# Optimization experiments

Measured on AMD Instinct MI355X. Metric: run time of the kernel, lower is better.

## Reference

```python
import jax, jax.numpy as jnp
import numpy as np

UNITS = 1024
N_CLASSES = 41
SUBSAMPLE = 4
KERNEL = 3
FEAT = 256


def setup_inputs() -> dict:
    key = jax.random.key(0)
    ks = jax.random.split(key, 12)
    B, T, F, U, C = 32, 1000, FEAT, UNITS, N_CLASSES
    s = lambda k, shape, sc: jax.random.normal(k, shape, dtype=jnp.float32) * sc
    return {
        "x": jax.random.normal(ks[0], (B, T, F), dtype=jnp.float32),
        # depthwise conv kernel: (width, 1, channels) for WIO with groups=C
        "conv_w": s(ks[1], (KERNEL, 1, F), 0.1),
        "h0_init": s(ks[2], (1, U), 0.05),
        "w0_x": s(ks[3], (F, 3 * U), 1.0 / np.sqrt(F)),
        "w0_h": s(ks[4], (U, 3 * U), 1.0 / np.sqrt(U)),
        "b0": jnp.zeros((2, 3 * U), dtype=jnp.float32),
        "w1_x": s(ks[5], (U, 3 * U), 1.0 / np.sqrt(U)),
        "w1_h": s(ks[6], (U, 3 * U), 1.0 / np.sqrt(U)),
        "b1": jnp.zeros((2, 3 * U), dtype=jnp.float32),
        "dense_w": s(ks[7], (U, C), 1.0 / np.sqrt(U)),
        "dense_b": jnp.zeros((C,), dtype=jnp.float32),
    }


def _depthwise_conv1d(x, w):
    # x: [B, T, C], w: [K, 1, C]; SAME padding, groups = C, relu, no bias
    C = x.shape[-1]
    y = jax.lax.conv_general_dilated(
        x, w, window_strides=(1,), padding="SAME",
        dimension_numbers=("NWC", "WIO", "NWC"), feature_group_count=C)
    return jax.nn.relu(y)


def _gru_layer(x, h0, Wx, Wh, b):
    # Keras GRU v2 (reset_after=True), gate order z, r, h.
    # x: [B, T, F]; h0: [B, U]; Wx: [F, 3U]; Wh: [U, 3U]; b: [2, 3U]
    xproj = jnp.einsum("btf,fg->btg", x, Wx) + b[0]  # [B, T, 3U]
    br = b[1]

    def step(h, xp):
        rec = h @ Wh + br  # [B, 3U]
        xz, xr, xh = jnp.split(xp, 3, axis=-1)
        rz, rr, rh = jnp.split(rec, 3, axis=-1)
        z = jax.nn.sigmoid(xz + rz)
        r = jax.nn.sigmoid(xr + rr)
        hh = jnp.tanh(xh + r * rh)
        hn = z * h + (1.0 - z) * hh
        return hn, hn

    _, ys = jax.lax.scan(step, h0, jnp.swapaxes(xproj, 0, 1))  # [T, B, U]
    return jnp.swapaxes(ys, 0, 1)


def reference(x, conv_w, h0_init, w0_x, w0_h, b0, w1_x, w1_h, b1, dense_w, dense_b):
    B = x.shape[0]
    U = w0_h.shape[0]
    h = _depthwise_conv1d(x, conv_w)
    # layer 0: learned initial state tiled over batch
    h = _gru_layer(h, jnp.tile(h0_init, (B, 1)), w0_x, w0_h, b0)
    # subsample after layer nLayers-2 == 0
    h = h[:, ::SUBSAMPLE, :]
    # layer 1: zero initial state (Keras default when initial_state is None)
    h = _gru_layer(h, jnp.zeros((B, U), dtype=x.dtype), w1_x, w1_h, b1)
    return h @ dense_w + dense_b  # [B, T//4, nClasses]
```

## Files before the change

kernel.cpp:

```cpp
#include <hip/hip_runtime.h>

typedef unsigned int u32;
typedef unsigned long long u64;
typedef unsigned short u16;
typedef __attribute__((ext_vector_type(8))) short short8;
typedef __attribute__((ext_vector_type(4))) float f32x4;
typedef __attribute__((ext_vector_type(4))) unsigned int u32x4;

#define MFMA(a,b,c) __builtin_amdgcn_mfma_f32_16x16x32_bf16((a),(b),(c),0,0,0)
#define ALOAD32(p)    __hip_atomic_load((p), __ATOMIC_RELAXED, __HIP_MEMORY_SCOPE_AGENT)
#define ASTORE32(p,v) __hip_atomic_store((p),(v), __ATOMIC_RELAXED, __HIP_MEMORY_SCOPE_AGENT)

__device__ __forceinline__ float bf2f(u32 b){ union{u32 u; float f;} v; v.u = b<<16; return v.f; }
__device__ __forceinline__ u16 f2bf(float f){ union{float f; u32 u;} v; v.f = f; u32 u = v.u;
  return (u16)((u + 0x7fffu + ((u>>16)&1u)) >> 16); }
__device__ __forceinline__ u32 pack_f(float v){
  u16 hi = f2bf(v); u16 lo = f2bf(v - bf2f(hi)); return (u32)hi | ((u32)lo<<16); }

__device__ __forceinline__ void unpack8(uint4 a, uint4 b, short8& hi, short8& lo){
  u32 w[8] = {a.x,a.y,a.z,a.w,b.x,b.y,b.z,b.w};
#pragma unroll
  for (int j=0;j<8;++j){ hi[j] = (short)(w[j] & 0xffffu); lo[j] = (short)(w[j] >> 16); }
}
__device__ __forceinline__ void unpackh4(u32x4 a, short8& hi){
#pragma unroll
  for (int i=0;i<4;++i){ hi[2*i] = (short)(a[i] & 0xffffu); hi[2*i+1] = (short)(a[i] >> 16); }
}

constexpr size_t OFF_Y    = 0;
constexpr size_t OFF_SUB  = 32768000;
constexpr size_t OFF_W0IH = 65536000;
constexpr size_t OFF_W0IL = 73400320;
constexpr size_t OFF_W1XH = 81264640;
constexpr size_t OFF_W1XL = 87556096;
constexpr size_t OFF_W1HH = 93847552;
constexpr size_t OFF_W1HL = 100139008;
constexpr size_t OFF_HB0  = 106430464;
constexpr size_t OFF_HB1  = 106692608;
constexpr size_t OFF_FL0  = 106954752;
constexpr size_t OFF_FL1  = 106955776;
constexpr size_t WS_NEED  = 106956800;

__global__ void build_frags(const float* __restrict__ W, u16* __restrict__ fhi,
                            u16* __restrict__ flo, int K){
  const int KT = K >> 8;
  size_t total = (size_t)K * 12 * 256;
  for (size_t i = (size_t)blockIdx.x*blockDim.x + threadIdx.x; i < total;
       i += (size_t)gridDim.x*blockDim.x){
    int j = (int)(i & 7); size_t r = i >> 3;
    int c = (int)(r % 12); r /= 12;
    int kseg = (int)(r & 3); r >>= 2;
    int kt = (int)(r % KT); r /= KT;
    int kq = (int)(r & 7); r >>= 3;
    int wg = (int)r;
    int k = kq*(K>>3) + kt*32 + kseg*8 + j;
    int col = (c>>2)*1024 + wg*4 + (c&3);
    float v = W[(size_t)k*3072 + col];
    u16 hi = f2bf(v);
    u16 lo = f2bf(v - bf2f(hi));
    fhi[i] = hi; flo[i] = lo;
  }
}

__global__ void build_w0img(const float* __restrict__ w0x, const float* __restrict__ w0h,
                            u16* __restrict__ imgH, u16* __restrict__ imgL){
  for (size_t i = (size_t)blockIdx.x*blockDim.x + threadIdx.x; i < 128ull*30720ull;
       i += (size_t)gridDim.x*blockDim.x){
    int wg = (int)(i / 30720), e = (int)(i % 30720);
    int k, col; const float* src;
    if (e < 4096){
      int blk=e>>9, r=e&511, kseg=r>>7, c=(r>>3)&15, j=r&7;
      k = blk*32 + kseg*8 + j;
      col = (c<8) ? (wg*8+c) : (1024 + wg*8 + c-8); src = w0x;
    } else if (e < 20480){
      int e2=e-4096, blk=e2>>9, r=e2&511, kseg=r>>7, c=(r>>3)&15, j=r&7;
      k = blk*32 + kseg*8 + j;
      col = (c<8) ? (wg*8+c) : (1024 + wg*8 + c-8); src = w0h;
    } else if (e < 24576){
      int e2=e-20480, blk=e2>>9, r=e2&511, kseg=r>>7, c=(r>>3)&15, j=r&7;
      k = blk*32 + kseg*8 + j;
      if (c < 8){ col = 2048 + wg*8 + c;     src = w0x; }
      else      { col = 2048 + wg*8 + c - 8; src = w0h; }
    } else {
      int e2=e-24576, blk=e2>>8, r=e2&255, kseg=r>>6, c=(r>>3)&7, j=r&7;
      k = 256 + blk*32 + kseg*8 + j;
      col = 2048 + wg*8 + c; src = w0h;
    }
    float v = src[(size_t)k*3072 + col];
    u16 hi = f2bf(v);
    imgH[i] = hi; imgL[i] = f2bf(v - bf2f(hi));
  }
}

__global__ void init_state(const float* __restrict__ h0, u32* hb0, u32* hb1,
                           int* f0, int* f1){
  int i = blockIdx.x*blockDim.x + threadIdx.x;
  if (i < 256){ f0[i]=0; f1[i]=0; }
  if (i < 16384){
    int p = i & 511;
    u32 v = (u32)f2bf(h0[2*p]) | ((u32)f2bf(h0[2*p+1]) << 16);
    hb0[i] = v;
    hb1[i] = 0u;
  }
}

__global__ void conv_pack(const float* __restrict__ x, const float* __restrict__ cw,
                          u32* __restrict__ yp){
  for (size_t i = (size_t)blockIdx.x*blockDim.x + threadIdx.x; i < 8192000ull;
       i += (size_t)gridDim.x*blockDim.x){
    int f = (int)(i & 255); int b = (int)((i>>8)&31); int t = (int)(i>>13);
    const float* xb = x + ((size_t)b*1000 + t)*256 + f;
    float acc = xb[0]*cw[256+f];
    if (t > 0)   acc += xb[-256]*cw[f];
    if (t < 999) acc += xb[256]*cw[512+f];
    acc = fmaxf(acc, 0.0f);
    yp[i] = pack_f(acc);
  }
}

__global__ __launch_bounds__(512, 1)
void gru8s_persist(const u32* __restrict__ xin,
                   const u16* __restrict__ imgH, const u16* __restrict__ imgL,
                   const float* __restrict__ bias,
                   u32* hbuf, int* flags, u32* out_pack)
{
  __shared__ u16 WIMG[45056];
  __shared__ float exch[128*33];
  __shared__ float harr[128];
  __shared__ int hready[32];

  const int tid  = threadIdx.x;
  const int wg   = blockIdx.x;
  const int g    = wg >> 7;
  const int wid  = wg & 127;
  const int lane = tid & 63;
  const int wave = tid >> 6;
  const int kq   = wave;
  const int lo16 = lane & 15, hi16 = lane >> 4;
  const int lane_off = hi16*128 + lo16*8;
  const int hsel = (kq >= 4) ? 16 : 0;

  {
    const u64* sH = (const u64*)(imgH + (size_t)wid*30720);
    const u64* sL = (const u64*)(imgL + (size_t)wid*30720 + 4096);
    u64* dH = (u64*)WIMG;
    u64* dL = (u64*)(WIMG + 24576);
    for (int i = tid; i < 6144; i += 512) dH[i] = sH[i];
    for (int i = tid; i < 5120; i += 512) dL[i] = sL[i];
    if (tid < 32) hready[tid] = 0;
    if (tid < 128){
      u16 hv = ((const u16*)hbuf)[g*16384 + (tid>>3)*1024 + wid*8 + (tid&7)];
      harr[tid] = bf2f((u32)hv);
    }
  }
  __syncthreads();

  const u16* zrx_h  = &WIMG[kq*512 + lane_off];
  const u16* zrxg_l = imgL + (size_t)wid*30720 + kq*512 + lane_off;
  const u16* zrh_h  = &WIMG[4096 + kq*2048 + lane_off];
  const u16* hhx_h  = &WIMG[20480 + kq*512 + lane_off];
  const bool hhLds  = (kq < 2);
  const u16* hhb_h; const u16* hhb_l; int hhstride;
  if (hhLds){
    hhb_h = &WIMG[20480 + kq*2048 + lane_off]; hhb_l = hhb_h + 20480; hhstride = 512;
  } else {
    size_t go = (size_t)wid*30720 + 24576 + (size_t)(kq-2)*1024 + hi16*64
              + ((lo16 >= 8) ? (lo16-8)*8 : 0);
    hhb_h = imgH + go; hhb_l = imgL + go; hhstride = 256;
  }

  const int gs = tid >> 3, gu = tid & 7, eu = wid*8 + gu;
  const float zb  = bias[eu]        + bias[3072 + eu];
  const float rbv = bias[1024 + eu] + bias[4096 + eu];
  const float hxb = bias[2048 + eu];
  const float hrb = bias[5120 + eu];

  for (int t = 0; t < 1000; ++t) {
    const int cur = t & 1, nxt = cur ^ 1;
    f32x4 aZR = (f32x4){0.f,0.f,0.f,0.f};
    f32x4 aHX = (f32x4){0.f,0.f,0.f,0.f};
    f32x4 aHR = (f32x4){0.f,0.f,0.f,0.f};
    {
      const u32* xr = xin + ((size_t)t*32 + g*16 + lo16)*256 + kq*32 + hi16*8;
      uint4 a0 = *(const uint4*)xr;
      uint4 a1 = *(const uint4*)(xr + 4);
      short8 ahi, alo; unpack8(a0, a1, ahi, alo);
      short8 b1h = *(const short8*)zrx_h, b1l = *(const short8*)zrxg_l;
      short8 b2h = *(const short8*)hhx_h, b2l = *(const short8*)(hhx_h + 20480);
      aZR = MFMA(ahi,b1h,aZR); aZR = MFMA(alo,b1h,aZR); aZR = MFMA(ahi,b1l,aZR);
      aHX = MFMA(ahi,b2h,aHX); aHX = MFMA(alo,b2h,aHX); aHX = MFMA(ahi,b2l,aHX);
    }
    if (t > 0) {
      if (wave == 0) {
        int f0;
        do { f0 = ALOAD32(flags + g*128 + lane); } while (__all(f0 >= t) == 0);
        asm volatile("" ::: "memory");
        if (lane == 0) ((volatile int*)hready)[0] = t;
      } else if (wave == 1) {
        int f1;
        do { f1 = ALOAD32(flags + g*128 + 64 + lane); } while (__all(f1 >= t) == 0);
        asm volatile("" ::: "memory");
        if (lane == 0) ((volatile int*)hready)[16] = t;
      }
      while (((volatile int*)hready)[hsel] < t) { }
      asm volatile("" ::: "memory");
    }
    {
      const u32* hrow = hbuf + cur*16384 + g*8192 + lo16*512 + kq*64 + hi16*4;
      u32x4 qa, qb, qc, qd;
      asm volatile(
        "global_load_dwordx4 %0, %4, off sc0 sc1\n\t"
        "global_load_dwordx4 %1, %4, off offset:64 sc0 sc1\n\t"
        "global_load_dwordx4 %2, %4, off offset:128 sc0 sc1\n\t"
        "global_load_dwordx4 %3, %4, off offset:192 sc0 sc1\n\t"
        "s_waitcnt vmcnt(0)"
        : "=&v"(qa), "=&v"(qb), "=&v"(qc), "=&v"(qd)
        : "v"(hrow)
        : "memory");
      short8 ah0, ah1, ah2, ah3;
      unpackh4(qa, ah0); unpackh4(qb, ah1); unpackh4(qc, ah2); unpackh4(qd, ah3);
      {
        short8 b1h = *(const short8*)(zrh_h + 0*512);
        short8 b1l = *(const short8*)(zrh_h + 0*512 + 20480);
        short8 b2h = *(const short8*)(hhb_h + 0*hhstride);
        short8 b2l = *(const short8*)(hhb_l + 0*hhstride);
        aZR = MFMA(ah0,b1h,aZR); aZR = MFMA(ah0,b1l,aZR);
        aHR = MFMA(ah0,b2h,aHR); aHR = MFMA(ah0,b2l,aHR);
      }
      {
        short8 b1h = *(const short8*)(zrh_h + 1*512);
        short8 b1l = *(const short8*)(zrh_h + 1*512 + 20480);
        short8 b2h = *(const short8*)(hhb_h + 1*hhstride);
        short8 b2l = *(const short8*)(hhb_l + 1*hhstride);
        aZR = MFMA(ah1,b1h,aZR); aZR = MFMA(ah1,b1l,aZR);
        aHR = MFMA(ah1,b2h,aHR); aHR = MFMA(ah1,b2l,aHR);
      }
      {
        short8 b1h = *(const short8*)(zrh_h + 2*512);
        short8 b1l = *(const short8*)(zrh_h + 2*512 + 20480);
        short8 b2h = *(const short8*)(hhb_h + 2*hhstride);
        short8 b2l = *(const short8*)(hhb_l + 2*hhstride);
        aZR = MFMA(ah2,b1h,aZR); aZR = MFMA(ah2,b1l,aZR);
        aHR = MFMA(ah2,b2h,aHR); aHR = MFMA(ah2,b2l,aHR);
      }
      {
        short8 b1h = *(const short8*)(zrh_h + 3*512);
        short8 b1l = *(const short8*)(zrh_h + 3*512 + 20480);
        short8 b2h = *(const short8*)(hhb_h + 3*hhstride);
        short8 b2l = *(const short8*)(hhb_l + 3*hhstride);
        aZR = MFMA(ah3,b1h,aZR); aZR = MFMA(ah3,b1l,aZR);
        aHR = MFMA(ah3,b2h,aHR); aHR = MFMA(ah3,b2l,aHR);
      }
    }
    {
      const int bb = hi16*4;
#pragma unroll
      for (int r4 = 0; r4 < 4; ++r4){
        exch[(kq*16 + bb + r4)*33 + lo16]      = aZR[r4];
        exch[(kq*16 + bb + r4)*33 + 16 + lo16] = (lo16 < 8) ? aHX[r4] : aHR[r4];
      }
    }
    __syncthreads();
    u32 pk_out = 0;
    if (tid < 128) {
      float zp=0.f, rp=0.f, xh=0.f, rh=0.f;
#pragma unroll
      for (int k8 = 0; k8 < 8; ++k8){
        const float* e = &exch[(k8*16 + gs)*33];
        zp += e[gu]; rp += e[8+gu]; xh += e[16+gu]; rh += e[24+gu];
      }
      float z = 1.f/(1.f + __expf(-(zp + zb)));
      float r = 1.f/(1.f + __expf(-(rp + rbv)));
      float pre = xh + hxb + r*(rh + hrb);
      float ex = __expf(-2.f*fabsf(pre));
      float th = (1.f - ex)/(1.f + ex);
      float hh = copysignf(th, pre);
      float hn = z*harr[tid] + (1.f - z)*hh;
      harr[tid] = hn;
      pk_out = pack_f(hn);
      int pk16 = (int)(pk_out & 0xffffu);
      int prt  = __shfl_xor(pk16, 1);
      if ((tid & 1) == 0) {
        u32 pair = (u32)pk16 | ((u32)prt << 16);
        ASTORE32(hbuf + nxt*16384 + g*8192 + gs*512 + wid*4 + (gu>>1), pair);
      }
    }
    asm volatile("s_waitcnt vmcnt(0)" ::: "memory");
    __syncthreads();
    if (tid == 0)
      ASTORE32(flags + g*128 + wid, t+1);
    if (tid < 128) {
      if ((t & 3) == 0)
        out_pack[((size_t)(t>>2)*32 + g*16 + gs)*1024 + eu] = pk_out;
    }
  }
}

template<int LAYER>
__global__ __launch_bounds__(1024, 1)
void gru_persist(const u32* __restrict__ xin,
                 const u16* __restrict__ wxf_hi, const u16* __restrict__ wxf_lo,
                 const u16* __restrict__ whf_hi, const u16* __restrict__ whf_lo,
                 const float* __restrict__ bias,
                 u32* hbuf, int* flags, u32* out_pack)
{
  constexpr int T   = (LAYER==0) ? 1000 : 250;
  constexpr int KX  = (LAYER==0) ? 256 : 1024;
  constexpr int KTX = KX >> 8;
  __shared__ u16 WxHi[8*KTX*512], WxLo[8*KTX*512];
  __shared__ u16 WhHi[8*4*512],  WhLo[8*4*512];
  __shared__ float exch[8*32*18];
  __shared__ float harr[128];
  __shared__ int hready[32];

  const int tid  = threadIdx.x;
  const int wg   = blockIdx.x;
  const int lane = tid & 63;
  const int wave = tid >> 6;
  const int m    = wave & 1;
  const int kq   = wave >> 1;
  const int u0   = wg * 4;
  const int lo16 = lane & 15, hi16 = lane >> 4;
  const int lane_off = hi16*128 + lo16*8;
  const int hsel = (kq >= 4) ? 16 : 0;

  {
    for (int i = tid; i < 8*KTX*512/4; i += 1024){ ((u64*)WxHi)[i]=0; ((u64*)WxLo)[i]=0; }
    for (int i = tid; i < 8*4*512/4;  i += 1024){ ((u64*)WhHi)[i]=0; ((u64*)WhLo)[i]=0; }
    if (tid < 32) hready[tid] = 0;
  }
  __syncthreads();
  {
    const u16* bx_hi = wxf_hi + (size_t)wg*KX*12;
    const u16* bx_lo = wxf_lo + (size_t)wg*KX*12;
    const u16* bh_hi = whf_hi + (size_t)wg*1024*12;
    const u16* bh_lo = whf_lo + (size_t)wg*1024*12;
    for (int i = tid; i < 8*KTX*48; i += 1024){
      int c = i % 12; int r = i/12; int kseg = r & 3; r >>= 2;
      int kt = r % KTX; int kqq = r / KTX;
      int ldsoff = ((kqq*KTX+kt)*4+kseg)*128 + c*8;
      *(short8*)&WxHi[ldsoff] = *(const short8*)&bx_hi[(size_t)i*8];
      *(short8*)&WxLo[ldsoff] = *(const short8*)&bx_lo[(size_t)i*8];
    }
    for (int i = tid; i < 8*4*48; i += 1024){
      int c = i % 12; int r = i/12; int kseg = r & 3; r >>= 2;
      int kt = r & 3; int kqq = r >> 2;
      int cm = (c < 8) ? c : (c + 4);
      int ldsoff = ((kqq*4+kt)*4+kseg)*128 + cm*8;
      *(short8*)&WhHi[ldsoff] = *(const short8*)&bh_hi[(size_t)i*8];
      *(short8*)&WhLo[ldsoff] = *(const short8*)&bh_lo[(size_t)i*8];
    }
    if (tid < 128){
      u16 hv = ((const u16*)hbuf)[(tid>>2)*1024 + u0 + (tid&3)];
      harr[tid] = bf2f((u32)hv);
    }
  }
  __syncthreads();

  const int eb = tid >> 2, eu_l = tid & 3, eu = u0 + eu_l;
  const float zb  = bias[eu]        + bias[3072 + eu];
  const float rbv = bias[1024 + eu] + bias[4096 + eu];
  const float hxb = bias[2048 + eu];
  const float hrb = bias[5120 + eu];

  for (int t = 0; t < T; ++t) {
    const int cur = t & 1, nxt = cur ^ 1;
    f32x4 xacc = (f32x4){0.f,0.f,0.f,0.f};
    f32x4 racc = (f32x4){0.f,0.f,0.f,0.f};
    {
      const u32* xrow = xin + ((size_t)t*32 + 16*m + lo16)*KX + kq*(KX>>3) + hi16*8;
#pragma unroll
      for (int kt = 0; kt < KTX; ++kt) {
        uint4 a0 = *(const uint4*)(xrow + kt*32);
        uint4 a1 = *(const uint4*)(xrow + kt*32 + 4);
        short8 ahi, alo; unpack8(a0, a1, ahi, alo);
        short8 bhi = *(const short8*)&WxHi[(kq*KTX+kt)*512 + lane_off];
        short8 blo = *(const short8*)&WxLo[(kq*KTX+kt)*512 + lane_off];
        xacc = MFMA(ahi, bhi, xacc);
        xacc = MFMA(alo, bhi, xacc);
        xacc = MFMA(ahi, blo, xacc);
      }
    }
    if (t > 0) {
      if (wave == 0) {
        int f0, f1;
        do { f0 = ALOAD32(flags + lane); f1 = ALOAD32(flags + 64 + lane); }
        while (!__all(f0 >= t && f1 >= t));
        asm volatile("" ::: "memory");
        if (lane == 0) ((volatile int*)hready)[0] = t;
      } else if (wave == 1) {
        int f2, f3;
        do { f2 = ALOAD32(flags + 128 + lane); f3 = ALOAD32(flags + 192 + lane); }
        while (!__all(f2 >= t && f3 >= t));
        asm volatile("" ::: "memory");
        if (lane == 0) ((volatile int*)hready)[16] = t;
      }
      while (((volatile int*)hready)[hsel] < t) { }
      asm volatile("" ::: "memory");
    }
    {
      const u32* hrow = hbuf + cur*16384 + (16*m + lo16)*512 + kq*64 + hi16*4;
      u32x4 qa, qb, qc, qd;
      asm volatile(
        "global_load_dwordx4 %0, %4, off sc0 sc1\n\t"
        "global_load_dwordx4 %1, %4, off offset:64 sc0 sc1\n\t"
        "global_load_dwordx4 %2, %4, off offset:128 sc0 sc1\n\t"
        "global_load_dwordx4 %3, %4, off offset:192 sc0 sc1\n\t"
        "s_waitcnt vmcnt(0)"
        : "=&v"(qa), "=&v"(qb), "=&v"(qc), "=&v"(qd)
        : "v"(hrow)
        : "memory");
      short8 ah0, ah1, ah2, ah3;
      unpackh4(qa, ah0); unpackh4(qb, ah1); unpackh4(qc, ah2); unpackh4(qd, ah3);
      {
        short8 bhi = *(const short8*)&WhHi[(kq*4+0)*512 + lane_off];
        short8 blo = *(const short8*)&WhLo[(kq*4+0)*512 + lane_off];
        racc = MFMA(ah0, bhi, racc); racc = MFMA(ah0, blo, racc);
      }
      {
        short8 bhi = *(const short8*)&WhHi[(kq*4+1)*512 + lane_off];
        short8 blo = *(const short8*)&WhLo[(kq*4+1)*512 + lane_off];
        racc = MFMA(ah1, bhi, racc); racc = MFMA(ah1, blo, racc);
      }
      {
        short8 bhi = *(const short8*)&WhHi[(kq*4+2)*512 + lane_off];
        short8 blo = *(const short8*)&WhLo[(kq*4+2)*512 + lane_off];
        racc = MFMA(ah2, bhi, racc); racc = MFMA(ah2, blo, racc);
      }
      {
        short8 bhi = *(const short8*)&WhHi[(kq*4+3)*512 + lane_off];
        short8 blo = *(const short8*)&WhLo[(kq*4+3)*512 + lane_off];
        racc = MFMA(ah3, bhi, racc); racc = MFMA(ah3, blo, racc);
      }
    }
    {
      const int bb = 16*m + hi16*4;
#pragma unroll
      for (int r4 = 0; r4 < 4; ++r4)
        exch[(kq*32 + bb + r4)*18 + lo16] = xacc[r4] + racc[r4];
    }
    __syncthreads();
    u32 pk_out = 0;
    if (tid < 128) {
      float zp=0.f, rp=0.f, xh=0.f, rh=0.f;
#pragma unroll
      for (int qd = 0; qd < 8; ++qd) {
        const float* e = &exch[(qd*32 + eb)*18];
        zp += e[eu_l];
        rp += e[4 + eu_l];
        xh += e[8 + eu_l];
        rh += e[12 + eu_l];
      }
      float z = 1.f/(1.f + __expf(-(zp + zb)));
      float r = 1.f/(1.f + __expf(-(rp + rbv)));
      float pre = xh + hxb + r*(rh + hrb);
      float ex = __expf(-2.f*fabsf(pre));
      float th = (1.f - ex)/(1.f + ex);
      float hh = copysignf(th, pre);
      float hn = z*harr[tid] + (1.f - z)*hh;
      harr[tid] = hn;
      pk_out = pack_f(hn);
      int pk16 = (int)(pk_out & 0xffffu);
      int prt  = __shfl_xor(pk16, 1);
      if ((tid & 1) == 0) {
        u32 pair = (u32)pk16 | ((u32)prt << 16);
        ASTORE32(hbuf + nxt*16384 + eb*512 + wg*2 + (eu_l>>1), pair);
      }
    }
    asm volatile("s_waitcnt vmcnt(0)" ::: "memory");
    __syncthreads();
    if (tid == 0)
      ASTORE32(flags + wg, t+1);
    if (tid < 128) {
      if (LAYER==0) {
        if ((t & 3) == 0)
          out_pack[((size_t)(t>>2)*32 + eb)*1024 + u0 + eu_l] = pk_out;
      } else {
        out_pack[((size_t)t*32 + eb)*1024 + u0 + eu_l] = pk_out;
      }
    }
  }
}

__global__ __launch_bounds__(256, 1)
void dense_k(const u32* __restrict__ h2, const float* __restrict__ W,
             const float* __restrict__ bias, float* __restrict__ out){
  __shared__ float rows[32*1025];
  const int ts = blockIdx.x;
  const u32* src = h2 + (size_t)ts*32768;
  for (int i = threadIdx.x; i < 32768; i += 256){
    u32 p = src[i];
    rows[(i>>10)*1025 + (i&1023)] = bf2f(p & 0xffffu) + bf2f(p >> 16);
  }
  __syncthreads();
  const int b = threadIdx.x >> 3, cg = threadIdx.x & 7;
  float acc[6] = {0.f,0.f,0.f,0.f,0.f,0.f};
  for (int k = 0; k < 1024; ++k){
    float hv = rows[b*1025 + k];
    const float* wr = W + k*41;
#pragma unroll
    for (int j = 0; j < 6; ++j){ int c = cg + 8*j; if (c < 41) acc[j] += hv*wr[c]; }
  }
#pragma unroll
  for (int j = 0; j < 6; ++j){
    int c = cg + 8*j;
    if (c < 41) out[((size_t)b*250 + ts)*41 + c] = acc[j] + bias[c];
  }
}

extern "C" void kernel_launch(void* const* d_in, const int* in_sizes, int n_in,
                              void* d_out, int out_size, void* d_ws, size_t ws_size,
                              hipStream_t stream) {
  const float* x      = (const float*)d_in[0];
  const float* conv_w = (const float*)d_in[1];
  const float* h0i    = (const float*)d_in[2];
  const float* w0x    = (const float*)d_in[3];
  const float* w0h    = (const float*)d_in[4];
  const float* b0     = (const float*)d_in[5];
  const float* w1x    = (const float*)d_in[6];
  const float* w1h    = (const float*)d_in[7];
  const float* b1     = (const float*)d_in[8];
  const float* dw     = (const float*)d_in[9];
  const float* db     = (const float*)d_in[10];
  float* outp = (float*)d_out;

  if (ws_size < WS_NEED) return;

  char* ws = (char*)d_ws;
  u32* y_pack   = (u32*)(ws + OFF_Y);
  u32* out2     = (u32*)(ws + OFF_Y);
  u32* sub_pack = (u32*)(ws + OFF_SUB);
  u16* w0iH = (u16*)(ws + OFF_W0IH); u16* w0iL = (u16*)(ws + OFF_W0IL);
  u16* w1x_hi = (u16*)(ws + OFF_W1XH); u16* w1x_lo = (u16*)(ws + OFF_W1XL);
  u16* w1h_hi = (u16*)(ws + OFF_W1HH); u16* w1h_lo = (u16*)(ws + OFF_W1HL);
  u32* hb0 = (u32*)(ws + OFF_HB0);
  u32* hb1 = (u32*)(ws + OFF_HB1);
  int* fl0 = (int*)(ws + OFF_FL0);
  int* fl1 = (int*)(ws + OFF_FL1);

  init_state<<<64, 512, 0, stream>>>(h0i, hb0, hb1, fl0, fl1);
  build_w0img<<<2048, 256, 0, stream>>>(w0x, w0h, w0iH, w0iL);
  build_frags<<<2048, 256, 0, stream>>>(w1x, w1x_hi, w1x_lo, 1024);
  build_frags<<<2048, 256, 0, stream>>>(w1h, w1h_hi, w1h_lo, 1024);
  conv_pack<<<4096, 256, 0, stream>>>(x, conv_w, y_pack);

  gru8s_persist<<<256, 512, 0, stream>>>(y_pack, w0iH, w0iL, b0, hb0, fl0, sub_pack);
  gru_persist<1><<<256, 1024, 0, stream>>>(sub_pack, w1x_hi, w1x_lo, w1h_hi, w1h_lo,
                                           b1, hb1, fl1, out2);

  dense_k<<<250, 256, 0, stream>>>(out2, dw, db, outp);
}
```

Before: 5.990 ms.

## Repartition layer-0 GRU into 4 batch groups of 8 with 16 units per block

The layer-0 persistent GRU now splits the batch into four groups of 8 sequences, and each block owns 16 hidden units instead of 8. Z, R and H gates each get a full 16-column MFMA tile, and the weight image is rebuilt in a matching layout. Only the hi halves go to LDS; the lo halves are now always read from global memory. The intent is to cut the number of blocks each one synchronises with per step (64 instead of 128) and to raise per-block work. The cost is that half of each 16-row MFMA is wasted on duplicated batch rows and there is more global traffic for the lo weights.

```diff
diff --git a/kernel.cpp b/kernel.cpp
--- a/kernel.cpp
+++ b/kernel.cpp
@@ -64,28 +64,20 @@
 
 __global__ void build_w0img(const float* __restrict__ w0x, const float* __restrict__ w0h,
                             u16* __restrict__ imgH, u16* __restrict__ imgL){
-  for (size_t i = (size_t)blockIdx.x*blockDim.x + threadIdx.x; i < 128ull*30720ull;
+  for (size_t i = (size_t)blockIdx.x*blockDim.x + threadIdx.x; i < 64ull*61440ull;
        i += (size_t)gridDim.x*blockDim.x){
-    int wg = (int)(i / 30720), e = (int)(i % 30720);
-    int k, col; const float* src;
-    if (e < 4096){
-      int blk=e>>9, r=e&511, kseg=r>>7, c=(r>>3)&15, j=r&7;
-      k = blk*32 + kseg*8 + j;
-      col = (c<8) ? (wg*8+c) : (1024 + wg*8 + c-8); src = w0x;
-    } else if (e < 20480){
-      int e2=e-4096, blk=e2>>9, r=e2&511, kseg=r>>7, c=(r>>3)&15, j=r&7;
-      k = blk*32 + kseg*8 + j;
-      col = (c<8) ? (wg*8+c) : (1024 + wg*8 + c-8); src = w0h;
-    } else if (e < 24576){
-      int e2=e-20480, blk=e2>>9, r=e2&511, kseg=r>>7, c=(r>>3)&15, j=r&7;
-      k = blk*32 + kseg*8 + j;
-      if (c < 8){ col = 2048 + wg*8 + c;     src = w0x; }
-      else      { col = 2048 + wg*8 + c - 8; src = w0h; }
-    } else {
-      int e2=e-24576, blk=e2>>8, r=e2&255, kseg=r>>6, c=(r>>3)&7, j=r&7;
-      k = 256 + blk*32 + kseg*8 + j;
-      col = 2048 + wg*8 + c; src = w0h;
-    }
+    int wid = (int)(i / 61440), e = (int)(i % 61440);
+    int e2, colbase; const float* src;
+    if      (e < 4096) { e2 = e;         colbase = 0;    src = w0x; }
+    else if (e < 8192) { e2 = e - 4096;  colbase = 1024; src = w0x; }
+    else if (e < 24576){ e2 = e - 8192;  colbase = 0;    src = w0h; }
+    else if (e < 40960){ e2 = e - 24576; colbase = 1024; src = w0h; }
+    else if (e < 45056){ e2 = e - 40960; colbase = 2048; src = w0x; }
+    else               { e2 = e - 45056; colbase = 2048; src = w0h; }
+    int blk = e2 >> 9, r = e2 & 511;
+    int kseg = r >> 7, c = (r >> 3) & 15, j = r & 7;
+    int k = blk*32 + kseg*8 + j;
+    int col = colbase + wid*16 + c;
     float v = src[(size_t)k*3072 + col];
     u16 hi = f2bf(v);
     imgH[i] = hi; imgL[i] = f2bf(v - bf2f(hi));
@@ -119,57 +111,49 @@
 }
 
 __global__ __launch_bounds__(512, 1)
-void gru8s_persist(const u32* __restrict__ xin,
+void gru16_persist(const u32* __restrict__ xin,
                    const u16* __restrict__ imgH, const u16* __restrict__ imgL,
                    const float* __restrict__ bias,
                    u32* hbuf, int* flags, u32* out_pack)
 {
-  __shared__ u16 WIMG[45056];
-  __shared__ float exch[128*33];
+  __shared__ u16 WIMG[61440];
+  __shared__ float exch[8*8*66];
   __shared__ float harr[128];
   __shared__ int hready[32];
 
   const int tid  = threadIdx.x;
   const int wg   = blockIdx.x;
-  const int g    = wg >> 7;
-  const int wid  = wg & 127;
+  const int g    = wg >> 6;
+  const int wid  = wg & 63;
   const int lane = tid & 63;
   const int wave = tid >> 6;
   const int kq   = wave;
   const int lo16 = lane & 15, hi16 = lane >> 4;
   const int lane_off = hi16*128 + lo16*8;
   const int hsel = (kq >= 4) ? 16 : 0;
+  const int srow = lo16 & 7;
 
   {
-    const u64* sH = (const u64*)(imgH + (size_t)wid*30720);
-    const u64* sL = (const u64*)(imgL + (size_t)wid*30720 + 4096);
+    const u64* sH = (const u64*)(imgH + (size_t)wid*61440);
     u64* dH = (u64*)WIMG;
-    u64* dL = (u64*)(WIMG + 24576);
-    for (int i = tid; i < 6144; i += 512) dH[i] = sH[i];
-    for (int i = tid; i < 5120; i += 512) dL[i] = sL[i];
+    for (int i = tid; i < 15360; i += 512) dH[i] = sH[i];
     if (tid < 32) hready[tid] = 0;
     if (tid < 128){
-      u16 hv = ((const u16*)hbuf)[g*16384 + (tid>>3)*1024 + wid*8 + (tid&7)];
+      u16 hv = ((const u16*)hbuf)[g*8192 + (tid>>4)*1024 + wid*16 + (tid&15)];
       harr[tid] = bf2f((u32)hv);
     }
   }
   __syncthreads();
 
-  const u16* zrx_h  = &WIMG[kq*512 + lane_off];
-  const u16* zrxg_l = imgL + (size_t)wid*30720 + kq*512 + lane_off;
-  const u16* zrh_h  = &WIMG[4096 + kq*2048 + lane_off];
-  const u16* hhx_h  = &WIMG[20480 + kq*512 + lane_off];
-  const bool hhLds  = (kq < 2);
-  const u16* hhb_h; const u16* hhb_l; int hhstride;
-  if (hhLds){
-    hhb_h = &WIMG[20480 + kq*2048 + lane_off]; hhb_l = hhb_h + 20480; hhstride = 512;
-  } else {
-    size_t go = (size_t)wid*30720 + 24576 + (size_t)(kq-2)*1024 + hi16*64
-              + ((lo16 >= 8) ? (lo16-8)*8 : 0);
-    hhb_h = imgH + go; hhb_l = imgL + go; hhstride = 256;
-  }
-
-  const int gs = tid >> 3, gu = tid & 7, eu = wid*8 + gu;
+  const u16* gLo  = imgL + (size_t)wid*61440;
+  const u16* zx_h = &WIMG[kq*512 + lane_off];          const u16* zx_l = gLo + kq*512 + lane_off;
+  const u16* rx_h = &WIMG[4096 + kq*512 + lane_off];   const u16* rx_l = gLo + 4096 + kq*512 + lane_off;
+  const u16* zh_h = &WIMG[8192 + kq*2048 + lane_off];  const u16* zh_l = gLo + 8192 + kq*2048 + lane_off;
+  const u16* rh_h = &WIMG[24576 + kq*2048 + lane_off]; const u16* rh_l = gLo + 24576 + kq*2048 + lane_off;
+  const u16* xh_h = &WIMG[40960 + kq*512 + lane_off];  const u16* xh_l = gLo + 40960 + kq*512 + lane_off;
+  const u16* hh_h = &WIMG[45056 + kq*2048 + lane_off]; const u16* hh_l = gLo + 45056 + kq*2048 + lane_off;
+
+  const int gs = tid >> 4, gu = tid & 15, eu = wid*16 + gu;
   const float zb  = bias[eu]        + bias[3072 + eu];
   const float rbv = bias[1024 + eu] + bias[4096 + eu];
   const float hxb = bias[2048 + eu];
@@ -177,28 +161,31 @@
 
   for (int t = 0; t < 1000; ++t) {
     const int cur = t & 1, nxt = cur ^ 1;
-    f32x4 aZR = (f32x4){0.f,0.f,0.f,0.f};
+    f32x4 aZ  = (f32x4){0.f,0.f,0.f,0.f};
+    f32x4 aR  = (f32x4){0.f,0.f,0.f,0.f};
     f32x4 aHX = (f32x4){0.f,0.f,0.f,0.f};
     f32x4 aHR = (f32x4){0.f,0.f,0.f,0.f};
     {
-      const u32* xr = xin + ((size_t)t*32 + g*16 + lo16)*256 + kq*32 + hi16*8;
+      const u32* xr = xin + ((size_t)t*32 + g*8 + srow)*256 + kq*32 + hi16*8;
       uint4 a0 = *(const uint4*)xr;
       uint4 a1 = *(const uint4*)(xr + 4);
       short8 ahi, alo; unpack8(a0, a1, ahi, alo);
-      short8 b1h = *(const short8*)zrx_h, b1l = *(const short8*)zrxg_l;
-      short8 b2h = *(const short8*)hhx_h, b2l = *(const short8*)(hhx_h + 20480);
-      aZR = MFMA(ahi,b1h,aZR); aZR = MFMA(alo,b1h,aZR); aZR = MFMA(ahi,b1l,aZR);
-      aHX = MFMA(ahi,b2h,aHX); aHX = MFMA(alo,b2h,aHX); aHX = MFMA(ahi,b2l,aHX);
+      short8 bzh = *(const short8*)zx_h, bzl = *(const short8*)zx_l;
+      short8 brh = *(const short8*)rx_h, brl = *(const short8*)rx_l;
+      short8 bxh = *(const short8*)xh_h, bxl = *(const short8*)xh_l;
+      aZ  = MFMA(ahi,bzh,aZ);  aZ  = MFMA(alo,bzh,aZ);  aZ  = MFMA(ahi,bzl,aZ);
+      aR  = MFMA(ahi,brh,aR);  aR  = MFMA(alo,brh,aR);  aR  = MFMA(ahi,brl,aR);
+      aHX = MFMA(ahi,bxh,aHX); aHX = MFMA(alo,bxh,aHX); aHX = MFMA(ahi,bxl,aHX);
     }
     if (t > 0) {
       if (wave == 0) {
         int f0;
-        do { f0 = ALOAD32(flags + g*128 + lane); } while (__all(f0 >= t) == 0);
+        do { f0 = ALOAD32(flags + g*64 + (lane & 31)); } while (__all(f0 >= t) == 0);
         asm volatile("" ::: "memory");
         if (lane == 0) ((volatile int*)hready)[0] = t;
       } else if (wave == 1) {
         int f1;
-        do { f1 = ALOAD32(flags + g*128 + 64 + lane); } while (__all(f1 >= t) == 0);
+        do { f1 = ALOAD32(flags + g*64 + 32 + (lane & 31)); } while (__all(f1 >= t) == 0);
         asm volatile("" ::: "memory");
         if (lane == 0) ((volatile int*)hready)[16] = t;
       }
@@ -206,7 +193,7 @@
       asm volatile("" ::: "memory");
     }
     {
-      const u32* hrow = hbuf + cur*16384 + g*8192 + lo16*512 + kq*64 + hi16*4;
+      const u32* hrow = hbuf + cur*16384 + g*4096 + srow*512 + kq*64 + hi16*4;
       u32x4 qa, qb, qc, qd;
       asm volatile(
         "global_load_dwordx4 %0, %4, off sc0 sc1\n\t"
@@ -219,45 +206,27 @@
         : "memory");
       short8 ah0, ah1, ah2, ah3;
       unpackh4(qa, ah0); unpackh4(qb, ah1); unpackh4(qc, ah2); unpackh4(qd, ah3);
-      {
-        short8 b1h = *(const short8*)(zrh_h + 0*512);
-        short8 b1l = *(const short8*)(zrh_h + 0*512 + 20480);
-        short8 b2h = *(const short8*)(hhb_h + 0*hhstride);
-        short8 b2l = *(const short8*)(hhb_l + 0*hhstride);
-        aZR = MFMA(ah0,b1h,aZR); aZR = MFMA(ah0,b1l,aZR);
-        aHR = MFMA(ah0,b2h,aHR); aHR = MFMA(ah0,b2l,aHR);
-      }
-      {
-        short8 b1h = *(const short8*)(zrh_h + 1*512);
-        short8 b1l = *(const short8*)(zrh_h + 1*512 + 20480);
-        short8 b2h = *(const short8*)(hhb_h + 1*hhstride);
-        short8 b2l = *(const short8*)(hhb_l + 1*hhstride);
-        aZR = MFMA(ah1,b1h,aZR); aZR = MFMA(ah1,b1l,aZR);
-        aHR = MFMA(ah1,b2h,aHR); aHR = MFMA(ah1,b2l,aHR);
-      }
-      {
-        short8 b1h = *(const short8*)(zrh_h + 2*512);
-        short8 b1l = *(const short8*)(zrh_h + 2*512 + 20480);
-        short8 b2h = *(const short8*)(hhb_h + 2*hhstride);
-        short8 b2l = *(const short8*)(hhb_l + 2*hhstride);
-        aZR = MFMA(ah2,b1h,aZR); aZR = MFMA(ah2,b1l,aZR);
-        aHR = MFMA(ah2,b2h,aHR); aHR = MFMA(ah2,b2l,aHR);
-      }
-      {
-        short8 b1h = *(const short8*)(zrh_h + 3*512);
-        short8 b1l = *(const short8*)(zrh_h + 3*512 + 20480);
-        short8 b2h = *(const short8*)(hhb_h + 3*hhstride);
-        short8 b2l = *(const short8*)(hhb_l + 3*hhstride);
-        aZR = MFMA(ah3,b1h,aZR); aZR = MFMA(ah3,b1l,aZR);
-        aHR = MFMA(ah3,b2h,aHR); aHR = MFMA(ah3,b2l,aHR);
+#pragma unroll
+      for (int kt = 0; kt < 4; ++kt){
+        short8 ah = (kt==0)?ah0:(kt==1)?ah1:(kt==2)?ah2:ah3;
+        short8 bzh = *(const short8*)(zh_h + kt*512), bzl = *(const short8*)(zh_l + kt*512);
+        short8 brh = *(const short8*)(rh_h + kt*512), brl = *(const short8*)(rh_l + kt*512);
+        short8 bhh = *(const short8*)(hh_h + kt*512), bhl = *(const short8*)(hh_l + kt*512);
+        aZ  = MFMA(ah,bzh,aZ);  aZ  = MFMA(ah,bzl,aZ);
+        aR  = MFMA(ah,brh,aR);  aR  = MFMA(ah,brl,aR);
+        aHR = MFMA(ah,bhh,aHR); aHR = MFMA(ah,bhl,aHR);
       }
     }
     {
-      const int bb = hi16*4;
-#pragma unroll
-      for (int r4 = 0; r4 < 4; ++r4){
-        exch[(kq*16 + bb + r4)*33 + lo16]      = aZR[r4];
-        exch[(kq*16 + bb + r4)*33 + 16 + lo16] = (lo16 < 8) ? aHX[r4] : aHR[r4];
+      if (hi16 < 2) {
+#pragma unroll
+        for (int r4 = 0; r4 < 4; ++r4){
+          float* e = &exch[(kq*8 + hi16*4 + r4)*66];
+          e[lo16]      = aZ[r4];
+          e[16 + lo16] = aR[r4];
+          e[32 + lo16] = aHX[r4];
+          e[48 + lo16] = aHR[r4];
+        }
       }
     }
     __syncthreads();
@@ -266,8 +235,8 @@
       float zp=0.f, rp=0.f, xh=0.f, rh=0.f;
 #pragma unroll
       for (int k8 = 0; k8 < 8; ++k8){
-        const float* e = &exch[(k8*16 + gs)*33];
-        zp += e[gu]; rp += e[8+gu]; xh += e[16+gu]; rh += e[24+gu];
+        const float* e = &exch[(k8*8 + gs)*66];
+        zp += e[gu]; rp += e[16+gu]; xh += e[32+gu]; rh += e[48+gu];
       }
       float z = 1.f/(1.f + __expf(-(zp + zb)));
       float r = 1.f/(1.f + __expf(-(rp + rbv)));
@@ -282,16 +251,16 @@
       int prt  = __shfl_xor(pk16, 1);
       if ((tid & 1) == 0) {
         u32 pair = (u32)pk16 | ((u32)prt << 16);
-        ASTORE32(hbuf + nxt*16384 + g*8192 + gs*512 + wid*4 + (gu>>1), pair);
+        ASTORE32(hbuf + nxt*16384 + g*4096 + gs*512 + wid*8 + (gu>>1), pair);
       }
     }
     asm volatile("s_waitcnt vmcnt(0)" ::: "memory");
     __syncthreads();
     if (tid == 0)
-      ASTORE32(flags + g*128 + wid, t+1);
+      ASTORE32(flags + g*64 + wid, t+1);
     if (tid < 128) {
       if ((t & 3) == 0)
-        out_pack[((size_t)(t>>2)*32 + g*16 + gs)*1024 + eu] = pk_out;
+        out_pack[((size_t)(t>>2)*32 + g*8 + gs)*1024 + eu] = pk_out;
     }
   }
 }
@@ -544,7 +513,7 @@
   build_frags<<<2048, 256, 0, stream>>>(w1h, w1h_hi, w1h_lo, 1024);
   conv_pack<<<4096, 256, 0, stream>>>(x, conv_w, y_pack);
 
-  gru8s_persist<<<256, 512, 0, stream>>>(y_pack, w0iH, w0iL, b0, hb0, fl0, sub_pack);
+  gru16_persist<<<256, 512, 0, stream>>>(y_pack, w0iH, w0iL, b0, hb0, fl0, sub_pack);
   gru_persist<1><<<256, 1024, 0, stream>>>(sub_pack, w1x_hi, w1x_lo, w1h_hi, w1h_lo,
                                            b1, hb1, fl1, out2);
 
```

After: 5.962 ms. Within noise of the previous version (-0.5%).
